# Kernel tuning notes

Hardware: AMD Instinct MI355X
Metric: run time of the kernel (lower is better)

The kernel has to match this reference:

```python
import jax, jax.numpy as jnp
import numpy as np


def setup_inputs() -> dict:
    key = jax.random.key(0)
    k1, k2 = jax.random.split(key)
    x = jax.random.normal(k1, (16, 1, 2048, 2048), dtype=jnp.float32)
    weight = jax.random.normal(k2, (1, 1, 3, 3), dtype=jnp.float32)  # Conv2d(1,1,3) weight, no bias
    den = jnp.ones((1,), dtype=jnp.float32)  # module-level global den = [1.0]
    return {"x": x, "weight": weight, "den": den}


def reference(x, weight, den):
    # kx = cat(den, [1.0], flip(den)) -> separable FIR taps; with den=[1.0], kx=[1,1,1].
    kx = jnp.concatenate([den, jnp.ones((1,), dtype=x.dtype), den[::-1]])  # [3]
    # The unfold + broadcast-mul + group-gather + kx/ky matmuls collapse (grp=1) to:
    #   out[b,co,h,w] = sum_{ci,i,j} kx[i]*kx[j]*weight[co,ci,i,j]*x_pad[b,ci,h+i,w+j]
    # i.e. a standard 3x3 stride-1 pad-1 conv with weight scaled by outer(kx,kx).
    eff_w = weight * (kx[:, None] * kx[None, :])  # [Cout, Cin, 3, 3]
    out = jax.lax.conv_general_dilated(
        x, eff_w,
        window_strides=(1, 1),
        padding=((1, 1), (1, 1)),
        dimension_numbers=("NCHW", "OIHW", "NCHW"),
    )
    return out
```

## Files before the change

kernel.cpp:

```cpp
#include <hip/hip_runtime.h>


#define IMG_W 2048
#define IMG_H 2048
#define BATCH 16
#define RPT 8
#define WCHUNKS (IMG_W / 4)
#define ROWGRPS (IMG_H / RPT)
#define NTHREADS (WCHUNKS * ROWGRPS * BATCH)
#define NBLOCKS (NTHREADS / 256)
#define NXCD 8

typedef float f4 __attribute__((ext_vector_type(4)));

__global__ __launch_bounds__(256) void conv3x3_kernel(
    const float* __restrict__ x,
    const float* __restrict__ weight,
    const float* __restrict__ den,
    float* __restrict__ out)
{
    const int bid = (int)(blockIdx.x % NXCD) * (NBLOCKS / NXCD)
                  + (int)(blockIdx.x / NXCD);
    const int tid    = bid * 256 + (int)threadIdx.x;
    const int wchunk = tid & (WCHUNKS - 1);
    const int rowgrp = (tid >> 9) & (ROWGRPS - 1);
    const int b      = tid >> 17;

    const float* xb = x   + (size_t)b * IMG_H * IMG_W;
    float*       ob = out + (size_t)b * IMG_H * IMG_W;
    const int w0 = wchunk * 4;
    const int h0 = rowgrp * RPT;
    const bool has_l = (w0 > 0);
    const bool has_r = (w0 + 4 < IMG_W);

    auto load_row = [&](int h, float v[6]) {
        if (h < 0 || h >= IMG_H) {
#pragma unroll
            for (int i = 0; i < 6; ++i) v[i] = 0.0f;
            return;
        }
        const float* r = xb + (size_t)h * IMG_W + w0;
        const f4 c = *(const f4*)r;
        v[1] = c.x; v[2] = c.y; v[3] = c.z; v[4] = c.w;
        v[0] = has_l ? r[-1] : 0.0f;
        v[5] = has_r ? r[4]  : 0.0f;
    };

    float r[RPT + 2][6];
#pragma unroll
    for (int i = 0; i < RPT + 2; ++i)
        load_row(h0 - 1 + i, r[i]);

    const float d = den[0];
    const float k[3] = {d, 1.0f, d};
    float wgt[3][3];
#pragma unroll
    for (int i = 0; i < 3; ++i)
#pragma unroll
        for (int j = 0; j < 3; ++j)
            wgt[i][j] = weight[i * 3 + j] * k[i] * k[j];

#pragma unroll
    for (int rr = 0; rr < RPT; ++rr) {
        f4 o;
#pragma unroll
        for (int j = 0; j < 4; ++j) {
            o[j] = wgt[0][0]*r[rr  ][j] + wgt[0][1]*r[rr  ][j+1] + wgt[0][2]*r[rr  ][j+2]
                 + wgt[1][0]*r[rr+1][j] + wgt[1][1]*r[rr+1][j+1] + wgt[1][2]*r[rr+1][j+2]
                 + wgt[2][0]*r[rr+2][j] + wgt[2][1]*r[rr+2][j+1] + wgt[2][2]*r[rr+2][j+2];
        }
        __builtin_nontemporal_store(
            o, (f4*)(ob + (size_t)(h0 + rr) * IMG_W + w0));
    }
}

extern "C" void kernel_launch(void* const* d_in, const int* in_sizes, int n_in,
                              void* d_out, int out_size, void* d_ws, size_t ws_size,
                              hipStream_t stream) {
    const float* x      = (const float*)d_in[0];
    const float* weight = (const float*)d_in[1];
    const float* den    = (const float*)d_in[2];
    float*       out    = (float*)d_out;

    conv3x3_kernel<<<NBLOCKS, 256, 0, stream>>>(x, weight, den, out);
}
```

Baseline: 446.9 us.

## Share halo columns via wavefront shuffles and drop XCD block remapping

```diff
diff --git a/kernel.cpp b/kernel.cpp
--- a/kernel.cpp
+++ b/kernel.cpp
@@ -9,7 +9,6 @@
 #define ROWGRPS (IMG_H / RPT)
 #define NTHREADS (WCHUNKS * ROWGRPS * BATCH)
 #define NBLOCKS (NTHREADS / 256)
-#define NXCD 8
 
 typedef float f4 __attribute__((ext_vector_type(4)));
 
@@ -19,9 +18,8 @@
     const float* __restrict__ den,
     float* __restrict__ out)
 {
-    const int bid = (int)(blockIdx.x % NXCD) * (NBLOCKS / NXCD)
-                  + (int)(blockIdx.x / NXCD);
-    const int tid    = bid * 256 + (int)threadIdx.x;
+    const int tid    = (int)blockIdx.x * 256 + (int)threadIdx.x;
+    const int lane   = (int)threadIdx.x & 63;
     const int wchunk = tid & (WCHUNKS - 1);
     const int rowgrp = (tid >> 9) & (ROWGRPS - 1);
     const int b      = tid >> 17;
@@ -33,23 +31,21 @@
     const bool has_l = (w0 > 0);
     const bool has_r = (w0 + 4 < IMG_W);
 
-    auto load_row = [&](int h, float v[6]) {
+    f4    c[RPT + 2];
+    float le[RPT + 2], re[RPT + 2];
+#pragma unroll
+    for (int i = 0; i < RPT + 2; ++i) {
+        const int h = h0 - 1 + i;
+        le[i] = 0.0f; re[i] = 0.0f;
         if (h < 0 || h >= IMG_H) {
-#pragma unroll
-            for (int i = 0; i < 6; ++i) v[i] = 0.0f;
-            return;
+            c[i] = (f4)0.0f;
+            continue;
         }
         const float* r = xb + (size_t)h * IMG_W + w0;
-        const f4 c = *(const f4*)r;
-        v[1] = c.x; v[2] = c.y; v[3] = c.z; v[4] = c.w;
-        v[0] = has_l ? r[-1] : 0.0f;
-        v[5] = has_r ? r[4]  : 0.0f;
-    };
-
-    float r[RPT + 2][6];
-#pragma unroll
-    for (int i = 0; i < RPT + 2; ++i)
-        load_row(h0 - 1 + i, r[i]);
+        c[i] = *(const f4*)r;
+        if (lane == 0  && has_l) le[i] = r[-1];
+        if (lane == 63 && has_r) re[i] = r[4];
+    }
 
     const float d = den[0];
     const float k[3] = {d, 1.0f, d};
@@ -60,18 +56,29 @@
         for (int j = 0; j < 3; ++j)
             wgt[i][j] = weight[i * 3 + j] * k[i] * k[j];
 
+    float v0[RPT + 2], v5[RPT + 2];
+#pragma unroll
+    for (int i = 0; i < RPT + 2; ++i) {
+        const float ls = __shfl_up(c[i].w, 1);
+        const float rs = __shfl_down(c[i].x, 1);
+        v0[i] = (lane == 0)  ? le[i] : ls;
+        v5[i] = (lane == 63) ? re[i] : rs;
+    }
+
+#define EL(i, k) ((k) == 0 ? v0[i] : ((k) == 5 ? v5[i] : c[i][(k) - 1]))
+
 #pragma unroll
     for (int rr = 0; rr < RPT; ++rr) {
         f4 o;
 #pragma unroll
         for (int j = 0; j < 4; ++j) {
-            o[j] = wgt[0][0]*r[rr  ][j] + wgt[0][1]*r[rr  ][j+1] + wgt[0][2]*r[rr  ][j+2]
-                 + wgt[1][0]*r[rr+1][j] + wgt[1][1]*r[rr+1][j+1] + wgt[1][2]*r[rr+1][j+2]
-                 + wgt[2][0]*r[rr+2][j] + wgt[2][1]*r[rr+2][j+1] + wgt[2][2]*r[rr+2][j+2];
+            o[j] = wgt[0][0]*EL(rr,   j) + wgt[0][1]*EL(rr,   j+1) + wgt[0][2]*EL(rr,   j+2)
+                 + wgt[1][0]*EL(rr+1, j) + wgt[1][1]*EL(rr+1, j+1) + wgt[1][2]*EL(rr+1, j+2)
+                 + wgt[2][0]*EL(rr+2, j) + wgt[2][1]*EL(rr+2, j+1) + wgt[2][2]*EL(rr+2, j+2);
         }
-        __builtin_nontemporal_store(
-            o, (f4*)(ob + (size_t)(h0 + rr) * IMG_W + w0));
+        *(f4*)(ob + (size_t)(h0 + rr) * IMG_W + w0) = o;
     }
+#undef EL
 }
 
 extern "C" void kernel_launch(void* const* d_in, const int* in_sizes, int n_in,
```

After: 435.5 us, median of 2. 1.03x faster.
